# Optimization experiments

Measured on AMD Instinct MI355X. Metric: run time of the kernel, lower is better.

The kernel has to match this reference:

```python
import jax, jax.numpy as jnp
import numpy as np

RES_H, RES_W = 64, 64
INV_SMOOTHNESS = 0.1
OFFSET = 0.5
LOSS_WEIGHT = 1.0


def bilinear_sample(mask, xs, ys):
    # mask: [IH, IW]; xs: [Wo]; ys: [Ho] in pixel coords -> [Ho, Wo]
    IH, IW = mask.shape
    x0 = jnp.floor(xs); y0 = jnp.floor(ys)
    wx = xs - x0; wy = ys - y0
    x0i = jnp.clip(x0.astype(jnp.int32), 0, IW - 1)
    x1i = jnp.clip(x0i + 1, 0, IW - 1)
    y0i = jnp.clip(y0.astype(jnp.int32), 0, IH - 1)
    y1i = jnp.clip(y0i + 1, 0, IH - 1)
    g = lambda yi, xi: mask[yi[:, None], xi[None, :]]
    return ((1 - wy)[:, None] * ((1 - wx)[None, :] * g(y0i, x0i) + wx[None, :] * g(y0i, x1i))
            + wy[:, None] * ((1 - wx)[None, :] * g(y1i, x0i) + wx[None, :] * g(y1i, x1i)))


def crop_and_resize(masks, boxes, Ho, Wo):
    # masks: [N, IH, IW]; boxes: [N, 4] xyxy -> binarized [N, Ho, Wo]
    def one(mask, box):
        x1, y1, x2, y2 = box[0], box[1], box[2], box[3]
        xs = x1 + (x2 - x1) * (jnp.arange(Wo, dtype=masks.dtype) + 0.5) / Wo - 0.5
        ys = y1 + (y2 - y1) * (jnp.arange(Ho, dtype=masks.dtype) + 0.5) / Ho - 0.5
        return bilinear_sample(mask, xs, ys)
    out = jax.vmap(one)(masks, boxes)
    return (out >= 0.5).astype(masks.dtype)


def rasterize_mask(verts, H, W, inv_s):
    # Soft polygon rasterization, MODE_MASK: sigmoid(sign * min_sq_dist * inv_s).
    # verts: [N, V, 2] (x, y) in pixel coords of the HxW grid.
    N, V, _ = verts.shape
    xs = jnp.arange(W, dtype=verts.dtype)
    ys = jnp.arange(H, dtype=verts.dtype)
    px = jnp.tile(xs, H)       # [P] with P = H*W
    py = jnp.repeat(ys, W)     # [P]
    p = jnp.stack([px, py], -1)  # [P, 2]
    a = verts                          # [N, V, 2]
    b = jnp.roll(verts, -1, axis=1)    # next vertex (closed polygon)
    ab = b - a                         # [N, V, 2]
    denom = jnp.sum(ab * ab, -1)       # [N, V]
    pa = p[None, :, None, :] - a[:, None, :, :]            # [N, P, V, 2]
    t = jnp.clip(jnp.einsum('npvc,nvc->npv', pa, ab) / (denom[:, None, :] + 1e-12), 0.0, 1.0)
    diff = pa - t[..., None] * ab[:, None, :, :]
    d2 = jnp.sum(diff * diff, -1)      # [N, P, V] squared point-to-segment dist
    d2min = jnp.min(d2, -1)            # [N, P]
    # even-odd crossing test for inside/outside sign
    ay = a[..., 1][:, None, :]; by = b[..., 1][:, None, :]     # [N, 1, V]
    pyb = py[None, :, None]
    cond = (ay > pyb) != (by > pyb)                             # [N, P, V]
    dy = ab[..., 1][:, None, :]
    safe_dy = jnp.where(dy == 0, 1.0, dy)
    xint = a[..., 0][:, None, :] + (pyb - ay) * ab[..., 0][:, None, :] / safe_dy
    crossings = jnp.sum((cond & (px[None, :, None] < xint)).astype(jnp.int32), -1)  # [N, P]
    sign = jnp.where(crossings % 2 == 1, 1.0, -1.0)
    return jax.nn.sigmoid(sign * d2min * inv_s).reshape(N, H, W)


def dice_loss(inp, tgt):
    n = inp.shape[0]
    smooth = 1.0
    iflat = inp.reshape(n, -1)
    tflat = tgt.reshape(n, -1)
    inter = jnp.sum(iflat * tflat, -1)
    losses = 1.0 - (2.0 * inter + smooth) / (jnp.sum(iflat, -1) + jnp.sum(tflat, -1) + smooth)
    return jnp.sum(losses) / n


def setup_inputs() -> dict:
    key = jax.random.key(0)
    k1, k2, k3, k4, k5, k6 = jax.random.split(key, 6)
    N, V, IMG = 128, 128, 512
    # star-shaped polygons (realistic contours) in image coords
    ctr = jax.random.uniform(k1, (N, 1, 2)) * (IMG * 0.6) + IMG * 0.2
    ang = jnp.linspace(0.0, 2.0 * jnp.pi, V, endpoint=False)
    rad = 20.0 + jax.random.uniform(k2, (N, V)) * 60.0
    preds = ctr + jnp.stack([rad * jnp.cos(ang), rad * jnp.sin(ang)], -1)  # [N, V, 2]
    # gt boxes xyxy
    x1y1 = jax.random.uniform(k3, (N, 2)) * (IMG * 0.3)
    wh = 50.0 + jax.random.uniform(k4, (N, 2)) * (IMG * 0.4)
    targets_bboxes = jnp.concatenate([x1y1, x1y1 + wh], -1)  # [N, 4]
    # gt full-image masks: random disks
    cb = jax.random.uniform(k5, (N, 2)) * IMG
    r = 30.0 + jax.random.uniform(k6, (N,)) * 100.0
    yy = jnp.arange(IMG, dtype=jnp.float32)[None, :, None]
    xx = jnp.arange(IMG, dtype=jnp.float32)[None, None, :]
    targets_masks = (((xx - cb[:, 0, None, None]) ** 2 + (yy - cb[:, 1, None, None]) ** 2)
                     < (r[:, None, None] ** 2)).astype(jnp.float32)  # [N, IMG, IMG]
    return {"preds": preds, "targets_masks": targets_masks, "targets_bboxes": targets_bboxes}


def reference(preds, targets_masks, targets_bboxes):
    # union bboxes of predicted polygon extent and gt bbox
    pmin = jnp.min(preds, axis=1)
    pmax = jnp.max(preds, axis=1)
    ub = jnp.concatenate([jnp.minimum(pmin, targets_bboxes[:, :2]),
                          jnp.maximum(pmax, targets_bboxes[:, 2:4])], -1)  # [N, 4]
    # crop + resize + binarize gt masks at the union boxes
    tgt = crop_and_resize(targets_masks, ub, RES_H, RES_W)  # [N, 64, 64]
    # normalize polygons into the (detached) union box
    ubd = jax.lax.stop_gradient(ub)
    normed = (preds - ubd[:, None, :2]) / (ubd[:, None, 2:4] - ubd[:, None, :2])
    verts = normed * float(RES_W) - OFFSET
    pred_masks = rasterize_mask(verts, RES_H, RES_W, INV_SMOOTHNESS)  # [N, 64, 64]
    pred_masks = jnp.clip(pred_masks, 1e-5, 0.99999)
    return dice_loss(pred_masks, tgt) * LOSS_WEIGHT
```

## Files before the change

### kernel.cpp

```cpp
#include <hip/hip_runtime.h>
#include <hip/hip_bf16.h>

#define NMASK 128
#define NV    128
#define IMG   512
#define RES   64
#define PB    8
#define NBLK  (NMASK*PB)
#define BT    256

#define EDGES_OFF 0
#define UB_OFF    131072
#define ACC_OFF   131584
#define FLAG_OFF  131968

__device__ __forceinline__ int clampi(int v, int lo, int hi) {
    return v < lo ? lo : (v > hi ? hi : v);
}

__device__ __forceinline__ int detect_bf16(const void* preds) {
    const __hip_bfloat16* pb = (const __hip_bfloat16*)preds;
    int lane = threadIdx.x & 63;
    float v = __bfloat162float(pb[2 * lane]);
    bool ok = (v >= 1.0f) && (v <= 600.0f);
    unsigned long long m = __ballot(ok);
    return (m == 0xFFFFFFFFFFFFFFFFULL) ? 1 : 0;
}

__device__ __forceinline__ float loadf(const void* p, long idx, int isb) {
    if (isb) return __bfloat162float(((const __hip_bfloat16*)p)[idx]);
    return ((const float*)p)[idx];
}

__global__ void __launch_bounds__(128) setup_kernel(
    const void* __restrict__ preds,
    const void* __restrict__ bboxes,
    float* __restrict__ ws)
{
    int n = blockIdx.x, t = threadIdx.x;
    int isb = detect_bf16(preds);

    float vx = loadf(preds, ((long)n*NV + t)*2 + 0, isb);
    float vy = loadf(preds, ((long)n*NV + t)*2 + 1, isb);

    float mnx = vx, mxx = vx, mny = vy, mxy = vy;
    for (int off = 32; off >= 1; off >>= 1) {
        mnx = fminf(mnx, __shfl_xor(mnx, off));
        mxx = fmaxf(mxx, __shfl_xor(mxx, off));
        mny = fminf(mny, __shfl_xor(mny, off));
        mxy = fmaxf(mxy, __shfl_xor(mxy, off));
    }
    __shared__ float r[2][4];
    int w = t >> 6;
    if ((t & 63) == 0) { r[w][0]=mnx; r[w][1]=mxx; r[w][2]=mny; r[w][3]=mxy; }
    __syncthreads();
    mnx = fminf(r[0][0], r[1][0]);
    mxx = fmaxf(r[0][1], r[1][1]);
    mny = fminf(r[0][2], r[1][2]);
    mxy = fmaxf(r[0][3], r[1][3]);

    float bx1 = loadf(bboxes, n*4 + 0, isb);
    float by1 = loadf(bboxes, n*4 + 1, isb);
    float bx2 = loadf(bboxes, n*4 + 2, isb);
    float by2 = loadf(bboxes, n*4 + 3, isb);
    float ux1 = fminf(mnx, bx1), uy1 = fminf(mny, by1);
    float ux2 = fmaxf(mxx, bx2), uy2 = fmaxf(mxy, by2);
    float sx = (float)RES / (ux2 - ux1);
    float sy = (float)RES / (uy2 - uy1);

    __shared__ float2 vn[NV];
    vn[t] = make_float2((vx - ux1)*sx - 0.5f, (vy - uy1)*sy - 0.5f);
    __syncthreads();

    float2 a = vn[t];
    float2 b = vn[(t + 1) & (NV - 1)];
    float abx = b.x - a.x, aby = b.y - a.y;
    float inv = 1.0f / (abx*abx + aby*aby + 1e-12f);
    float slope = abx / ((aby == 0.0f) ? 1.0f : aby);

    float4* eg = (float4*)(ws + EDGES_OFF + (size_t)n * NV * 8);
    eg[2*t]   = make_float4(a.x, a.y, abx, aby);
    eg[2*t+1] = make_float4(abx*inv, aby*inv, slope, b.y);

    if (t == 0) {
        ws[UB_OFF + n*4 + 0] = ux1;
        ws[UB_OFF + n*4 + 1] = uy1;
        ws[UB_OFF + n*4 + 2] = ux2;
        ws[UB_OFF + n*4 + 3] = uy2;
        ws[ACC_OFF + n*3 + 0] = 0.0f;
        ws[ACC_OFF + n*3 + 1] = 0.0f;
        ws[ACC_OFF + n*3 + 2] = 0.0f;
        if (n == 0) ((int*)ws)[FLAG_OFF] = isb;
    }
}

__global__ void __launch_bounds__(BT) MaskRasterizationLoss_2705829396671_kernel(
    const void* __restrict__ masks,
    const float4* __restrict__ edges,
    const float* __restrict__ meta,
    float* __restrict__ acc)
{
    int n    = blockIdx.x >> 3;
    int part = blockIdx.x & 7;
    int t    = threadIdx.x;

    const float4* eg = edges + (size_t)n * NV * 2;

    float ux1 = meta[UB_OFF + n*4 + 0], uy1 = meta[UB_OFF + n*4 + 1];
    float ux2 = meta[UB_OFF + n*4 + 2], uy2 = meta[UB_OFF + n*4 + 3];
    int isb = ((const int*)meta)[FLAG_OFF];

    int p0 = part * 512 + t * 2;
    float py  = (float)(p0 >> 6);
    float pxb = (float)(p0 & 63);
    float px1v = pxb + 1.0f;

    float d2m0 = 1e30f, d2m1 = 1e30f;
    int   cr0 = 0, cr1 = 0;

    #pragma unroll 8
    for (int v = 0; v < NV; ++v) {
        float4 eA = eg[2*v];
        float4 eB = eg[2*v+1];

        float pay  = py - eA.y;
        float q    = pay * eB.y;
        bool  cnd  = (eA.y > py) != (eB.w > py);
        float xint = fmaf(pay, eB.z, eA.x);

        {
            float pax = pxb - eA.x;
            float tt  = fmaf(pax, eB.x, q);
            tt = fminf(fmaxf(tt, 0.0f), 1.0f);
            float dx  = fmaf(-tt, eA.z, pax);
            float dyv = fmaf(-tt, eA.w, pay);
            float d2  = fmaf(dx, dx, dyv*dyv);
            d2m0 = fminf(d2m0, d2);
            cr0 += (cnd && (pxb < xint)) ? 1 : 0;
        }
        {
            float pax = px1v - eA.x;
            float tt  = fmaf(pax, eB.x, q);
            tt = fminf(fmaxf(tt, 0.0f), 1.0f);
            float dx  = fmaf(-tt, eA.z, pax);
            float dyv = fmaf(-tt, eA.w, pay);
            float d2  = fmaf(dx, dx, dyv*dyv);
            d2m1 = fminf(d2m1, d2);
            cr1 += (cnd && (px1v < xint)) ? 1 : 0;
        }
    }

    long mbase = (long)n * IMG * IMG;
    float invW = (ux2 - ux1) * (1.0f/(float)RES);
    float invH = (uy2 - uy1) * (1.0f/(float)RES);
    float ys = fmaf(py + 0.5f, invH, uy1) - 0.5f;
    float fy = floorf(ys), wy = ys - fy;
    int y0i = clampi((int)fy, 0, IMG-1);
    int y1i = clampi(y0i + 1, 0, IMG-1);

    float s_pred = 0.0f, s_tgt = 0.0f, s_int = 0.0f;
    #pragma unroll
    for (int k = 0; k < 2; ++k) {
        float px    = k ? px1v : pxb;
        float d2min = k ? d2m1 : d2m0;
        int   cross = k ? cr1  : cr0;

        float sgn = (cross & 1) ? 1.0f : -1.0f;
        float z = sgn * d2min * 0.1f;
        float sg = 1.0f / (1.0f + __expf(-z));
        sg = fminf(fmaxf(sg, 1e-5f), 0.99999f);

        float xs = fmaf(px + 0.5f, invW, ux1) - 0.5f;
        float fx = floorf(xs), wx = xs - fx;
        int x0i = clampi((int)fx, 0, IMG-1);
        int x1i = clampi(x0i + 1, 0, IMG-1);
        float g00 = loadf(masks, mbase + (long)y0i*IMG + x0i, isb);
        float g01 = loadf(masks, mbase + (long)y0i*IMG + x1i, isb);
        float g10 = loadf(masks, mbase + (long)y1i*IMG + x0i, isb);
        float g11 = loadf(masks, mbase + (long)y1i*IMG + x1i, isb);
        float bil = (1.0f-wy) * ((1.0f-wx)*g00 + wx*g01)
                  +        wy * ((1.0f-wx)*g10 + wx*g11);
        float tg = (bil >= 0.5f) ? 1.0f : 0.0f;

        s_pred += sg;
        s_tgt  += tg;
        s_int  += sg * tg;
    }

    for (int off = 32; off >= 1; off >>= 1) {
        s_pred += __shfl_xor(s_pred, off);
        s_tgt  += __shfl_xor(s_tgt,  off);
        s_int  += __shfl_xor(s_int,  off);
    }
    __shared__ float red[3][4];
    int wave = t >> 6;
    if ((t & 63) == 0) { red[0][wave]=s_pred; red[1][wave]=s_tgt; red[2][wave]=s_int; }
    __syncthreads();
    if (t == 0) {
        atomicAdd(&acc[n*3+0], red[0][0]+red[0][1]+red[0][2]+red[0][3]);
        atomicAdd(&acc[n*3+1], red[1][0]+red[1][1]+red[1][2]+red[1][3]);
        atomicAdd(&acc[n*3+2], red[2][0]+red[2][1]+red[2][2]+red[2][3]);
    }
}

__global__ void __launch_bounds__(128) finalize_kernel(
    const float* __restrict__ acc, void* __restrict__ out)
{
    int t = threadIdx.x;
    float sp = acc[t*3+0], st = acc[t*3+1], si = acc[t*3+2];
    float loss = 1.0f - (2.0f*si + 1.0f) / (sp + st + 1.0f);
    for (int off = 32; off >= 1; off >>= 1)
        loss += __shfl_xor(loss, off);
    __shared__ float tmp[2];
    if ((t & 63) == 0) tmp[t >> 6] = loss;
    __syncthreads();
    if (t == 0) {
        float L = (tmp[0] + tmp[1]) * (1.0f/128.0f);
        unsigned int fb = __float_as_uint(L);
        unsigned int r  = (fb + 0x7FFFu + ((fb >> 16) & 1u)) >> 16;
        ((unsigned int*)out)[0] = (r << 16) | r;
    }
}

extern "C" void kernel_launch(void* const* d_in, const int* in_sizes, int n_in,
                              void* d_out, int out_size, void* d_ws, size_t ws_size,
                              hipStream_t stream) {
    const void* preds  = d_in[0];
    const void* masks  = d_in[1];
    const void* bboxes = d_in[2];
    float* ws = (float*)d_ws;

    setup_kernel<<<NMASK, 128, 0, stream>>>(preds, bboxes, ws);
    MaskRasterizationLoss_2705829396671_kernel<<<NBLK, BT, 0, stream>>>(
        masks, (const float4*)(ws + EDGES_OFF), ws, ws + ACC_OFF);
    finalize_kernel<<<1, 128, 0, stream>>>(ws + ACC_OFF, d_out);
}
```

Baseline: 191.6 us.

## Cull polygon edges per row strip before distance and crossing loops

Each block first classifies the polygon's edges against its 8-row strip. It builds a shared list of edges whose bounding-box lower-bound squared distance is under a threshold, and a separate list of edges that span the strip vertically. The distance loop then runs only over near edges and the crossing-count loop only over spanning edges. This skips edges that cannot change the clipped sigmoid or the parity. The cost is a shared-memory prefilter with atomics, extra syncs, and a threshold that relies on the sigmoid clamp saturating.

Measured after the change: 198.8 us. 1.04x slower.

```diff
diff --git a/kernel.cpp b/kernel.cpp
--- a/kernel.cpp
+++ b/kernel.cpp
@@ -13,6 +13,8 @@
 #define UB_OFF    131072
 #define ACC_OFF   131584
 #define FLAG_OFF  131968
+
+#define CULL_D2 118.0f
 
 __device__ __forceinline__ int clampi(int v, int lo, int hi) {
     return v < lo ? lo : (v > hi ? hi : v);
@@ -115,19 +117,48 @@
     float pxb = (float)(p0 & 63);
     float px1v = pxb + 1.0f;
 
+    float Ylo = (float)(part * 8);
+    float Yhi = (float)(part * 8 + 7);
+
+    __shared__ unsigned short nearIdx[NV];
+    __shared__ unsigned short crossIdx[NV];
+    __shared__ int cnts[2];
+    if (t < 2) cnts[t] = 0;
+    __syncthreads();
+    if (t < NV) {
+        float4 eA = eg[2*t];
+        float4 eB = eg[2*t+1];
+        float bxv = eA.x + eA.z;
+        float xmn = fminf(eA.x, bxv), xmx = fmaxf(eA.x, bxv);
+        float ymn = fminf(eA.y, eB.w), ymx = fmaxf(eA.y, eB.w);
+        float dx = fmaxf(fmaxf(xmn - 63.0f, -xmx), 0.0f);
+        float dy = fmaxf(fmaxf(ymn - Yhi, Ylo - ymx), 0.0f);
+        float lb = fmaf(dx, dx, dy*dy);
+        if (lb < CULL_D2) {
+            int p = atomicAdd(&cnts[0], 1);
+            nearIdx[p] = (unsigned short)t;
+        }
+        bool nocross = (ymn > Yhi) || (ymx <= Ylo);
+        if (!nocross) {
+            int p = atomicAdd(&cnts[1], 1);
+            crossIdx[p] = (unsigned short)t;
+        }
+    }
+    __syncthreads();
+    int nNear  = __builtin_amdgcn_readfirstlane(cnts[0]);
+    int nCross = __builtin_amdgcn_readfirstlane(cnts[1]);
+
     float d2m0 = 1e30f, d2m1 = 1e30f;
     int   cr0 = 0, cr1 = 0;
 
-    #pragma unroll 8
-    for (int v = 0; v < NV; ++v) {
-        float4 eA = eg[2*v];
-        float4 eB = eg[2*v+1];
+    #pragma unroll 4
+    for (int i = 0; i < nNear; ++i) {
+        int idx = __builtin_amdgcn_readfirstlane((int)nearIdx[i]);
+        float4 eA = eg[2*idx];
+        float4 eB = eg[2*idx+1];
 
         float pay  = py - eA.y;
         float q    = pay * eB.y;
-        bool  cnd  = (eA.y > py) != (eB.w > py);
-        float xint = fmaf(pay, eB.z, eA.x);
-
         {
             float pax = pxb - eA.x;
             float tt  = fmaf(pax, eB.x, q);
@@ -136,7 +167,6 @@
             float dyv = fmaf(-tt, eA.w, pay);
             float d2  = fmaf(dx, dx, dyv*dyv);
             d2m0 = fminf(d2m0, d2);
-            cr0 += (cnd && (pxb < xint)) ? 1 : 0;
         }
         {
             float pax = px1v - eA.x;
@@ -146,8 +176,20 @@
             float dyv = fmaf(-tt, eA.w, pay);
             float d2  = fmaf(dx, dx, dyv*dyv);
             d2m1 = fminf(d2m1, d2);
-            cr1 += (cnd && (px1v < xint)) ? 1 : 0;
-        }
+        }
+    }
+
+    #pragma unroll 4
+    for (int i = 0; i < nCross; ++i) {
+        int idx = __builtin_amdgcn_readfirstlane((int)crossIdx[i]);
+        float4 eA = eg[2*idx];
+        float4 eB = eg[2*idx+1];
+
+        float pay  = py - eA.y;
+        bool  cnd  = (eA.y > py) != (eB.w > py);
+        float xint = fmaf(pay, eB.z, eA.x);
+        cr0 += (cnd && (pxb  < xint)) ? 1 : 0;
+        cr1 += (cnd && (px1v < xint)) ? 1 : 0;
     }
 
     long mbase = (long)n * IMG * IMG;
```
